# Kernel optimization log

Hardware: AMD Instinct MI355X
Metric: run time of the kernel (lower is better)

## Reference

```python
import jax, jax.numpy as jnp
import numpy as np

BETA = 0.25


def setup_inputs() -> dict:
    key = jax.random.key(0)
    k1, k2 = jax.random.split(key)
    x = jax.random.normal(k1, (64, 32, 32, 64), dtype=jnp.float32)
    # codebook stored as [embedding_dim, num_embeddings], as in the layer
    embeddings = jax.random.normal(k2, (64, 1024), dtype=jnp.float32) * 0.05
    return {"x": x, "embeddings": embeddings}


def reference(x, embeddings):
    input_shape = x.shape
    d = embeddings.shape[0]
    flat = x.reshape(-1, d)  # [N, D]

    sim = flat @ embeddings  # [N, K]
    distances = (
        jnp.sum(flat ** 2, axis=1, keepdims=True)
        + jnp.sum(embeddings ** 2, axis=0)
        - 2.0 * sim
    )
    encoding_indices = jnp.argmin(distances, axis=1)  # [N]

    # one_hot @ embeddings.T is mathematically a gather of codebook rows
    quantized = jnp.take(embeddings.T, encoding_indices, axis=0)  # [N, D]
    quantized = quantized.reshape(input_shape)

    commitment_loss = jnp.mean((jax.lax.stop_gradient(quantized) - x) ** 2)
    codebook_loss = jnp.mean((quantized - jax.lax.stop_gradient(x)) ** 2)
    loss = BETA * commitment_loss + codebook_loss

    # straight-through estimator
    quantized_st = x + jax.lax.stop_gradient(quantized - x)
    return quantized_st, loss
```

## Files before the change

kernel.cpp:

```cpp
#include <hip/hip_runtime.h>

#define D 64
#define K 1024
#define NPTS 65536
#define OUT_ELEMS (NPTS * D)
#define PAD4 17

typedef __bf16 bf16x8 __attribute__((ext_vector_type(8)));
typedef float  f32x4  __attribute__((ext_vector_type(4)));


static __device__ __forceinline__ void split1(float v, __bf16& h, __bf16& mid,
                                              __bf16& lo) {
    h = (__bf16)v;
    const float fh = (float)h;
    const float r1 = v - fh;
    mid = (__bf16)r1;
    const float fm = (float)mid;
    lo = (__bf16)(r1 - fm);
}

__global__ __launch_bounds__(256) void vq_prep(const float* __restrict__ emb,
                                               float* __restrict__ eT,
                                               float* __restrict__ enorm_h,
                                               __bf16* __restrict__ ebh,
                                               __bf16* __restrict__ ebm,
                                               __bf16* __restrict__ ebl,
                                               float* __restrict__ loss_out) {
    __shared__ float tile[64][65];
    const int t    = threadIdx.x;
    const int lane = t & 63;
    const int quad = t >> 6;
    const int k0   = blockIdx.x * 64;

#pragma unroll
    for (int i = 0; i < 16; ++i) {
        const int d = i * 4 + quad;
        tile[d][lane] = emb[d * K + k0 + lane];
    }
    __syncthreads();

    const int kk = t >> 2, c = t & 3;
    const int krow = k0 + kk;
#pragma unroll
    for (int j = 0; j < 16; ++j) {
        const int d = c * 16 + j;
        const float v = tile[d][kk];
        const int idx = krow * D + d;
        eT[idx] = v;
        __bf16 h, mid, lo;
        split1(v, h, mid, lo);
        ebh[idx] = h; ebm[idx] = mid; ebl[idx] = lo;
    }

    if (t < 64) {
        float s = __fmul_rn(tile[0][t], tile[0][t]);
        for (int dd = 1; dd < D; ++dd)
            s = __fadd_rn(s, __fmul_rn(tile[dd][t], tile[dd][t]));
        enorm_h[k0 + t] = 0.5f * s;
    }
    if (blockIdx.x == 0 && t == 0) *loss_out = 0.0f;
}

static __device__ __forceinline__ float sq8(float a, float b, float c, float d,
                                            float e, float f, float g, float h) {
    float r = __fmul_rn(a, a);
    r = __fadd_rn(r, __fmul_rn(b, b));
    r = __fadd_rn(r, __fmul_rn(c, c));
    r = __fadd_rn(r, __fmul_rn(d, d));
    r = __fadd_rn(r, __fmul_rn(e, e));
    r = __fadd_rn(r, __fmul_rn(f, f));
    r = __fadd_rn(r, __fmul_rn(g, g));
    r = __fadd_rn(r, __fmul_rn(h, h));
    return r;
}

#define PINF(v) asm volatile("" : "+v"(v))

#define MFMA(A, B, C) C = __builtin_amdgcn_mfma_f32_16x16x32_bf16(A, B, C, 0, 0, 0)

#define MKFRAG(FH, FM, FL, U0, U1) {                      \
    __bf16 h_, m_, l_;                                    \
    split1(U0.x, h_, m_, l_); FH[0]=h_; FM[0]=m_; FL[0]=l_; \
    split1(U0.y, h_, m_, l_); FH[1]=h_; FM[1]=m_; FL[1]=l_; \
    split1(U0.z, h_, m_, l_); FH[2]=h_; FM[2]=m_; FL[2]=l_; \
    split1(U0.w, h_, m_, l_); FH[3]=h_; FM[3]=m_; FL[3]=l_; \
    split1(U1.x, h_, m_, l_); FH[4]=h_; FM[4]=m_; FL[4]=l_; \
    split1(U1.y, h_, m_, l_); FH[5]=h_; FM[5]=m_; FL[5]=l_; \
    split1(U1.z, h_, m_, l_); FH[6]=h_; FM[6]=m_; FL[6]=l_; \
    split1(U1.w, h_, m_, l_); FH[7]=h_; FM[7]=m_; FL[7]=l_; }

static __device__ __forceinline__ void cp16(const void* gptr, void* lptr) {
    __builtin_amdgcn_global_load_lds(
        (const __attribute__((address_space(1))) void*)gptr,
        (__attribute__((address_space(3))) void*)lptr, 16, 0, 0);
}

__global__ __launch_bounds__(256, 2) void vq_main(const float* __restrict__ x,
        const float* __restrict__ eT, const float* __restrict__ enorm_h,
        const __bf16* __restrict__ ebh, const __bf16* __restrict__ ebm,
        const __bf16* __restrict__ ebl,
        float* __restrict__ out, float* __restrict__ loss_out) {
    __shared__ __align__(16) char smem[51712];
    float*  rpart = (float*)(smem + 12288);
    int*    swin  = (int*)(smem + 16384);
    float*  skey  = (float*)(smem + 16896);
    int*    sct   = (int*)(smem + 25088);
    float4* slab  = (float4*)(smem + 16896);

    const int t     = threadIdx.x;
    const int lane  = t & 63;
    const int w     = t >> 6;
    const int m     = lane & 15;
    const int quad  = lane >> 4;
    const int pbase = blockIdx.x * 128 + w * 32;

    const int n0   = lane >> 3;
    const int jj   = lane & 7;
    const int soff = n0 * 128 + (((jj - n0) & 7) << 4);
    const char* gsA = (w <= 1) ? (const char*)ebh : (const char*)ebm;
    const int   IA  = w & 1;
    const int   dA  = ((w <= 1) ? 0 : 2048) + IA * 1024;
    const int   sA  = soff + IA * 1024;
    const char* gsB = (const char*)ebl;
    const int   dB  = 4096 + w * 1024;
    const int   sB  = soff + w * 1024;

    const int o0 = (m * 8 + ((quad + m) & 7)) * 16;
    const int o1 = (m * 8 + ((4 + quad + m) & 7)) * 16;

    cp16(gsA + sA, smem + dA);
    if (w <= 1) cp16(gsB + sB, smem + dB);

    bf16x8 Ah00, Am00, Al00, Ah01, Am01, Al01;
    bf16x8 Ah10, Am10, Al10, Ah11, Am11, Al11;
#define LOADA(TT, HH, FH, FM, FL) {                                        \
    const float* px = x + ((size_t)(pbase + TT * 16 + m)) * D + HH * 32 + quad * 8; \
    const float4 u0 = *(const float4*)px;                                  \
    const float4 u1 = *(const float4*)(px + 4);                            \
    rpart[(w * 32 + TT * 16 + m) * 8 + (HH * 4 + quad)] =                  \
        sq8(u0.x, u0.y, u0.z, u0.w, u1.x, u1.y, u1.z, u1.w);               \
    MKFRAG(FH, FM, FL, u0, u1); }
    LOADA(0, 0, Ah00, Am00, Al00)
    LOADA(0, 1, Ah01, Am01, Al01)
    LOADA(1, 0, Ah10, Am10, Al10)
    LOADA(1, 1, Ah11, Am11, Al11)
#undef LOADA
    PINF(Ah00); PINF(Am00); PINF(Al00); PINF(Ah01); PINF(Am01); PINF(Al01);
    PINF(Ah10); PINF(Am10); PINF(Al10); PINF(Ah11); PINF(Am11); PINF(Al11);

    const float FINF = 3.402823466e38f;
    float bk00 = FINF, bk01 = FINF, bk02 = FINF, bk03 = FINF;
    float bk10 = FINF, bk11 = FINF, bk12 = FINF, bk13 = FINF;
    int   bc00 = 0, bc01 = 0, bc02 = 0, bc03 = 0;
    int   bc10 = 0, bc11 = 0, bc12 = 0, bc13 = 0;

#define TILE_BODY(BBOFF, CT, PRET, PREOFF) {                               \
    __syncthreads();             \
    const char* bb = smem + (BBOFF);                                       \
    const bf16x8 Bh0 = *(const bf16x8*)(bb + o0);                          \
    const bf16x8 Bh1 = *(const bf16x8*)(bb + o1);                          \
    const bf16x8 Bm0 = *(const bf16x8*)(bb + 2048 + o0);                   \
    const bf16x8 Bm1 = *(const bf16x8*)(bb + 2048 + o1);                   \
    const bf16x8 Bl0 = *(const bf16x8*)(bb + 4096 + o0);                   \
    const bf16x8 Bl1 = *(const bf16x8*)(bb + 4096 + o1);                   \
    cp16(gsA + (size_t)(PRET) * 2048 + sA, smem + (PREOFF) + dA);          \
    if (w <= 1) cp16(gsB + (size_t)(PRET) * 2048 + sB, smem + (PREOFF) + dB); \
    __builtin_amdgcn_sched_barrier(0);                \
    const float enh = enorm_h[(CT) * 16 + m];                              \
    f32x4 c0a = {0.f,0.f,0.f,0.f}, c0b = {0.f,0.f,0.f,0.f};                \
    f32x4 c1a = {0.f,0.f,0.f,0.f}, c1b = {0.f,0.f,0.f,0.f};                \
    MFMA(Ah00, Bh0, c0a); MFMA(Ah10, Bh0, c1a);                            \
    MFMA(Ah01, Bh1, c0b); MFMA(Ah11, Bh1, c1b);                            \
    MFMA(Am00, Bh0, c0a); MFMA(Am10, Bh0, c1a);                            \
    MFMA(Am01, Bh1, c0b); MFMA(Am11, Bh1, c1b);                            \
    MFMA(Ah00, Bm0, c0a); MFMA(Ah10, Bm0, c1a);                            \
    MFMA(Ah01, Bm1, c0b); MFMA(Ah11, Bm1, c1b);                            \
    MFMA(Am00, Bm0, c0a); MFMA(Am10, Bm0, c1a);                            \
    MFMA(Am01, Bm1, c0b); MFMA(Am11, Bm1, c1b);                            \
    MFMA(Ah00, Bl0, c0a); MFMA(Ah10, Bl0, c1a);                            \
    MFMA(Ah01, Bl1, c0b); MFMA(Ah11, Bl1, c1b);                            \
    MFMA(Al00, Bh0, c0a); MFMA(Al10, Bh0, c1a);                            \
    MFMA(Al01, Bh1, c0b); MFMA(Al11, Bh1, c1b);                            \
    const f32x4 c0 = c0a + c0b;                                            \
    const f32x4 c1 = c1a + c1b;                                            \
    { const float kv = enh - c0[0]; if (kv < bk00) { bk00 = kv; bc00 = (CT); } } \
    { const float kv = enh - c0[1]; if (kv < bk01) { bk01 = kv; bc01 = (CT); } } \
    { const float kv = enh - c0[2]; if (kv < bk02) { bk02 = kv; bc02 = (CT); } } \
    { const float kv = enh - c0[3]; if (kv < bk03) { bk03 = kv; bc03 = (CT); } } \
    { const float kv = enh - c1[0]; if (kv < bk10) { bk10 = kv; bc10 = (CT); } } \
    { const float kv = enh - c1[1]; if (kv < bk11) { bk11 = kv; bc11 = (CT); } } \
    { const float kv = enh - c1[2]; if (kv < bk12) { bk12 = kv; bc12 = (CT); } } \
    { const float kv = enh - c1[3]; if (kv < bk13) { bk13 = kv; bc13 = (CT); } } }

    for (int j = 0; j < 32; ++j) {
        const int ct0 = 2 * j;
        const int ct1 = 2 * j + 1;
        const int tp2 = (2 * j + 2) & 63;
        TILE_BODY(0,    ct0, ct1, 6144)
        TILE_BODY(6144, ct1, tp2, 0)
    }
#undef TILE_BODY

#define PUTC(TT, REG, BK, BC) {                                   \
    const int ploc = w * 32 + TT * 16 + quad * 4 + REG;           \
    skey[ploc * 16 + m] = BK; sct[ploc * 16 + m] = BC; }
    PUTC(0, 0, bk00, bc00) PUTC(0, 1, bk01, bc01)
    PUTC(0, 2, bk02, bc02) PUTC(0, 3, bk03, bc03)
    PUTC(1, 0, bk10, bc10) PUTC(1, 1, bk11, bc11)
    PUTC(1, 2, bk12, bc12) PUTC(1, 3, bk13, bc13)
#undef PUTC
    __syncthreads();

    if (t < 128) {
        const int p = t;
        const float* rp = rpart + p * 8;
        const float A = ((rp[0] + rp[1]) + (rp[2] + rp[3])) +
                        ((rp[4] + rp[5]) + (rp[6] + rp[7]));
        float fb = FINF;
        int   fi = 0;
#pragma unroll
        for (int c = 0; c < 16; ++c) {
            const float kv = skey[p * 16 + c];
            const int   iv = sct[p * 16 + c] * 16 + c;
            if (kv < fb || (kv == fb && iv < fi)) { fb = kv; fi = iv; }
        }
        swin[p] = fi;
        float lp = fmaf(2.0f, fb, A);
#pragma unroll
        for (int off = 32; off > 0; off >>= 1) lp += __shfl_down(lp, off, 64);
        if (lane == 0) atomicAdd(loss_out, lp * (1.25f / (float)OUT_ELEMS));
    }
    __syncthreads();

    {
        const int p = t >> 1, c = t & 1;
        const int fi = swin[p];
        const float4* qr = (const float4*)(eT + (size_t)fi * D) + c * 8;
        float4* dst = slab + p * PAD4 + c * 8;
#pragma unroll
        for (int j = 0; j < 8; ++j) dst[j] = qr[j];
    }
    __syncthreads();
    float4* og = (float4*)out + (size_t)blockIdx.x * 2048;
#pragma unroll
    for (int s = 0; s < 8; ++s) {
        const int f = s * 256 + t;
        og[f] = slab[(f >> 4) * PAD4 + (f & 15)];
    }
}

extern "C" void kernel_launch(void* const* d_in, const int* in_sizes, int n_in,
                              void* d_out, int out_size, void* d_ws, size_t ws_size,
                              hipStream_t stream) {
    const float* x   = (const float*)d_in[0];
    const float* emb = (const float*)d_in[1];
    float* out       = (float*)d_out;
    char*  ws        = (char*)d_ws;
    float*  eT       = (float*)ws;
    float*  enorm_h  = (float*)(ws + 262144);
    __bf16* ebh      = (__bf16*)(ws + 266240);
    __bf16* ebm      = (__bf16*)(ws + 397312);
    __bf16* ebl      = (__bf16*)(ws + 528384);
    float* loss_out  = out + OUT_ELEMS;

    vq_prep<<<dim3(K / 64), dim3(256), 0, stream>>>(emb, eT, enorm_h, ebh, ebm,
                                                    ebl, loss_out);
    vq_main<<<dim3(NPTS / 128), dim3(256), 0, stream>>>(x, eT, enorm_h, ebh,
                                                        ebm, ebl, out, loss_out);
}
```

Before: 123.5 us.

## Double waves per block, giving each wave 16 points instead of 32

New measurement: 122.5 us. Within noise of the previous version (-0.9%).

```diff
diff --git a/kernel.cpp b/kernel.cpp
--- a/kernel.cpp
+++ b/kernel.cpp
@@ -96,7 +96,7 @@
         (__attribute__((address_space(3))) void*)lptr, 16, 0, 0);
 }
 
-__global__ __launch_bounds__(256, 2) void vq_main(const float* __restrict__ x,
+__global__ __launch_bounds__(512, 4) void vq_main(const float* __restrict__ x,
         const float* __restrict__ eT, const float* __restrict__ enorm_h,
         const __bf16* __restrict__ ebh, const __bf16* __restrict__ ebm,
         const __bf16* __restrict__ ebl,
@@ -113,50 +113,42 @@
     const int w     = t >> 6;
     const int m     = lane & 15;
     const int quad  = lane >> 4;
-    const int pbase = blockIdx.x * 128 + w * 32;
+    const int pbase = blockIdx.x * 128 + w * 16;
 
     const int n0   = lane >> 3;
     const int jj   = lane & 7;
     const int soff = n0 * 128 + (((jj - n0) & 7) << 4);
-    const char* gsA = (w <= 1) ? (const char*)ebh : (const char*)ebm;
+    const char* gsA = (w < 2) ? (const char*)ebh
+                    : (w < 4) ? (const char*)ebm : (const char*)ebl;
     const int   IA  = w & 1;
-    const int   dA  = ((w <= 1) ? 0 : 2048) + IA * 1024;
+    const int   dA  = (w >> 1) * 2048 + IA * 1024;
     const int   sA  = soff + IA * 1024;
-    const char* gsB = (const char*)ebl;
-    const int   dB  = 4096 + w * 1024;
-    const int   sB  = soff + w * 1024;
 
     const int o0 = (m * 8 + ((quad + m) & 7)) * 16;
     const int o1 = (m * 8 + ((4 + quad + m) & 7)) * 16;
 
-    cp16(gsA + sA, smem + dA);
-    if (w <= 1) cp16(gsB + sB, smem + dB);
-
-    bf16x8 Ah00, Am00, Al00, Ah01, Am01, Al01;
-    bf16x8 Ah10, Am10, Al10, Ah11, Am11, Al11;
-#define LOADA(TT, HH, FH, FM, FL) {                                        \
-    const float* px = x + ((size_t)(pbase + TT * 16 + m)) * D + HH * 32 + quad * 8; \
+    if (w < 6) cp16(gsA + sA, smem + dA);
+
+    bf16x8 Ah0, Am0, Al0, Ah1, Am1, Al1;
+#define LOADA(HH, FH, FM, FL) {                                            \
+    const float* px = x + ((size_t)(pbase + m)) * D + HH * 32 + quad * 8;  \
     const float4 u0 = *(const float4*)px;                                  \
     const float4 u1 = *(const float4*)(px + 4);                            \
-    rpart[(w * 32 + TT * 16 + m) * 8 + (HH * 4 + quad)] =                  \
+    rpart[(w * 16 + m) * 8 + (HH * 4 + quad)] =                            \
         sq8(u0.x, u0.y, u0.z, u0.w, u1.x, u1.y, u1.z, u1.w);               \
     MKFRAG(FH, FM, FL, u0, u1); }
-    LOADA(0, 0, Ah00, Am00, Al00)
-    LOADA(0, 1, Ah01, Am01, Al01)
-    LOADA(1, 0, Ah10, Am10, Al10)
-    LOADA(1, 1, Ah11, Am11, Al11)
+    LOADA(0, Ah0, Am0, Al0)
+    LOADA(1, Ah1, Am1, Al1)
 #undef LOADA
-    PINF(Ah00); PINF(Am00); PINF(Al00); PINF(Ah01); PINF(Am01); PINF(Al01);
-    PINF(Ah10); PINF(Am10); PINF(Al10); PINF(Ah11); PINF(Am11); PINF(Al11);
+    PINF(Ah0); PINF(Am0); PINF(Al0); PINF(Ah1); PINF(Am1); PINF(Al1);
 
     const float FINF = 3.402823466e38f;
-    float bk00 = FINF, bk01 = FINF, bk02 = FINF, bk03 = FINF;
-    float bk10 = FINF, bk11 = FINF, bk12 = FINF, bk13 = FINF;
-    int   bc00 = 0, bc01 = 0, bc02 = 0, bc03 = 0;
-    int   bc10 = 0, bc11 = 0, bc12 = 0, bc13 = 0;
+    float bk0 = FINF, bk1 = FINF, bk2 = FINF, bk3 = FINF;
+    int   bc0 = 0, bc1 = 0, bc2 = 0, bc3 = 0;
 
 #define TILE_BODY(BBOFF, CT, PRET, PREOFF) {                               \
-    __syncthreads();             \
+    __syncthreads();   \
+    if (w < 6) cp16(gsA + (size_t)(PRET) * 2048 + sA, smem + (PREOFF) + dA); \
     const char* bb = smem + (BBOFF);                                       \
     const bf16x8 Bh0 = *(const bf16x8*)(bb + o0);                          \
     const bf16x8 Bh1 = *(const bf16x8*)(bb + o1);                          \
@@ -164,34 +156,19 @@
     const bf16x8 Bm1 = *(const bf16x8*)(bb + 2048 + o1);                   \
     const bf16x8 Bl0 = *(const bf16x8*)(bb + 4096 + o0);                   \
     const bf16x8 Bl1 = *(const bf16x8*)(bb + 4096 + o1);                   \
-    cp16(gsA + (size_t)(PRET) * 2048 + sA, smem + (PREOFF) + dA);          \
-    if (w <= 1) cp16(gsB + (size_t)(PRET) * 2048 + sB, smem + (PREOFF) + dB); \
-    __builtin_amdgcn_sched_barrier(0);                \
     const float enh = enorm_h[(CT) * 16 + m];                              \
-    f32x4 c0a = {0.f,0.f,0.f,0.f}, c0b = {0.f,0.f,0.f,0.f};                \
-    f32x4 c1a = {0.f,0.f,0.f,0.f}, c1b = {0.f,0.f,0.f,0.f};                \
-    MFMA(Ah00, Bh0, c0a); MFMA(Ah10, Bh0, c1a);                            \
-    MFMA(Ah01, Bh1, c0b); MFMA(Ah11, Bh1, c1b);                            \
-    MFMA(Am00, Bh0, c0a); MFMA(Am10, Bh0, c1a);                            \
-    MFMA(Am01, Bh1, c0b); MFMA(Am11, Bh1, c1b);                            \
-    MFMA(Ah00, Bm0, c0a); MFMA(Ah10, Bm0, c1a);                            \
-    MFMA(Ah01, Bm1, c0b); MFMA(Ah11, Bm1, c1b);                            \
-    MFMA(Am00, Bm0, c0a); MFMA(Am10, Bm0, c1a);                            \
-    MFMA(Am01, Bm1, c0b); MFMA(Am11, Bm1, c1b);                            \
-    MFMA(Ah00, Bl0, c0a); MFMA(Ah10, Bl0, c1a);                            \
-    MFMA(Ah01, Bl1, c0b); MFMA(Ah11, Bl1, c1b);                            \
-    MFMA(Al00, Bh0, c0a); MFMA(Al10, Bh0, c1a);                            \
-    MFMA(Al01, Bh1, c0b); MFMA(Al11, Bh1, c1b);                            \
-    const f32x4 c0 = c0a + c0b;                                            \
-    const f32x4 c1 = c1a + c1b;                                            \
-    { const float kv = enh - c0[0]; if (kv < bk00) { bk00 = kv; bc00 = (CT); } } \
-    { const float kv = enh - c0[1]; if (kv < bk01) { bk01 = kv; bc01 = (CT); } } \
-    { const float kv = enh - c0[2]; if (kv < bk02) { bk02 = kv; bc02 = (CT); } } \
-    { const float kv = enh - c0[3]; if (kv < bk03) { bk03 = kv; bc03 = (CT); } } \
-    { const float kv = enh - c1[0]; if (kv < bk10) { bk10 = kv; bc10 = (CT); } } \
-    { const float kv = enh - c1[1]; if (kv < bk11) { bk11 = kv; bc11 = (CT); } } \
-    { const float kv = enh - c1[2]; if (kv < bk12) { bk12 = kv; bc12 = (CT); } } \
-    { const float kv = enh - c1[3]; if (kv < bk13) { bk13 = kv; bc13 = (CT); } } }
+    f32x4 ca = {0.f,0.f,0.f,0.f}, cb = {0.f,0.f,0.f,0.f};                  \
+    MFMA(Ah0, Bh0, ca); MFMA(Ah1, Bh1, cb);                        \
+    MFMA(Am0, Bh0, ca); MFMA(Am1, Bh1, cb);                        \
+    MFMA(Ah0, Bm0, ca); MFMA(Ah1, Bm1, cb);                        \
+    MFMA(Am0, Bm0, ca); MFMA(Am1, Bm1, cb);                        \
+    MFMA(Ah0, Bl0, ca); MFMA(Ah1, Bl1, cb);                        \
+    MFMA(Al0, Bh0, ca); MFMA(Al1, Bh1, cb);                        \
+    const f32x4 c0 = ca + cb;                                              \
+    { const float kv = enh - c0[0]; if (kv < bk0) { bk0 = kv; bc0 = (CT); } } \
+    { const float kv = enh - c0[1]; if (kv < bk1) { bk1 = kv; bc1 = (CT); } } \
+    { const float kv = enh - c0[2]; if (kv < bk2) { bk2 = kv; bc2 = (CT); } } \
+    { const float kv = enh - c0[3]; if (kv < bk3) { bk3 = kv; bc3 = (CT); } } }
 
     for (int j = 0; j < 32; ++j) {
         const int ct0 = 2 * j;
@@ -202,13 +179,10 @@
     }
 #undef TILE_BODY
 
-#define PUTC(TT, REG, BK, BC) {                                   \
-    const int ploc = w * 32 + TT * 16 + quad * 4 + REG;           \
+#define PUTC(REG, BK, BC) {                                       \
+    const int ploc = w * 16 + quad * 4 + REG;                     \
     skey[ploc * 16 + m] = BK; sct[ploc * 16 + m] = BC; }
-    PUTC(0, 0, bk00, bc00) PUTC(0, 1, bk01, bc01)
-    PUTC(0, 2, bk02, bc02) PUTC(0, 3, bk03, bc03)
-    PUTC(1, 0, bk10, bc10) PUTC(1, 1, bk11, bc11)
-    PUTC(1, 2, bk12, bc12) PUTC(1, 3, bk13, bc13)
+    PUTC(0, bk0, bc0) PUTC(1, bk1, bc1) PUTC(2, bk2, bc2) PUTC(3, bk3, bc3)
 #undef PUTC
     __syncthreads();
 
@@ -234,18 +208,18 @@
     __syncthreads();
 
     {
-        const int p = t >> 1, c = t & 1;
+        const int p = t >> 2, c = t & 3;
         const int fi = swin[p];
-        const float4* qr = (const float4*)(eT + (size_t)fi * D) + c * 8;
-        float4* dst = slab + p * PAD4 + c * 8;
-#pragma unroll
-        for (int j = 0; j < 8; ++j) dst[j] = qr[j];
+        const float4* qr = (const float4*)(eT + (size_t)fi * D) + c * 4;
+        float4* dst = slab + p * PAD4 + c * 4;
+#pragma unroll
+        for (int j = 0; j < 4; ++j) dst[j] = qr[j];
     }
     __syncthreads();
     float4* og = (float4*)out + (size_t)blockIdx.x * 2048;
 #pragma unroll
-    for (int s = 0; s < 8; ++s) {
-        const int f = s * 256 + t;
+    for (int s = 0; s < 4; ++s) {
+        const int f = s * 512 + t;
         og[f] = slab[(f >> 4) * PAD4 + (f & 15)];
     }
 }
@@ -266,6 +240,6 @@
 
     vq_prep<<<dim3(K / 64), dim3(256), 0, stream>>>(emb, eT, enorm_h, ebh, ebm,
                                                     ebl, loss_out);
-    vq_main<<<dim3(NPTS / 128), dim3(256), 0, stream>>>(x, eT, enorm_h, ebh,
+    vq_main<<<dim3(NPTS / 128), dim3(512), 0, stream>>>(x, eT, enorm_h, ebh,
                                                         ebm, ebl, out, loss_out);
 }
```
